# Kernel optimization log

Measured on AMD Instinct MI355X. Metric: run time of the kernel, lower is better.

Reference implementation:

```python
import jax, jax.numpy as jnp
import numpy as np

B, V, E, L, D = 4, 64, 1024, 1024, 256  # batch, vertices, edges/graph, seq_len, d_model
DEG = E // V


def setup_inputs() -> dict:
    key = jax.random.key(0)
    k0, k1, k2, k3, k4, k5 = jax.random.split(key, 6)
    # fixed 16-regular graph, edges sorted by (src, dst) so that nonzero()
    # extraction order of the dense adjacency equals a gather at (src, dst)
    src = np.repeat(np.arange(V), DEG)
    dst = (src + 1 + np.tile(np.arange(DEG), V)) % V
    order = np.lexsort((dst, src))
    src, dst = src[order], dst[order]
    edge_index = jnp.asarray(np.stack([np.tile(src, B), np.tile(dst, B)]), dtype=jnp.int32)
    hidden_states = jax.random.normal(k0, (B * V, L, D), dtype=jnp.float32)
    edge_weight = jax.random.uniform(k1, (B * E,), dtype=jnp.float32, minval=0.1, maxval=1.0)
    s = 0.02
    Wq = jax.random.normal(k2, (D, D), dtype=jnp.float32) * s
    bq = jax.random.normal(k3, (D,), dtype=jnp.float32) * s
    Wk = jax.random.normal(k4, (D, D), dtype=jnp.float32) * s
    bk = jax.random.normal(k5, (D,), dtype=jnp.float32) * s
    attn_skip = jnp.float32(0.5)
    return {"hidden_states": hidden_states, "edge_index": edge_index, "edge_weight": edge_weight,
            "Wq": Wq, "bq": bq, "Wk": Wk, "bk": bk, "attn_skip": attn_skip}


def reference(hidden_states, edge_index, edge_weight, Wq, bq, Wk, bk, attn_skip):
    # broadcast static edge list / weights across time, as the torch repeat does
    ei = jnp.broadcast_to(edge_index[:, :, None], (2, B * E, L))
    ew = jnp.broadcast_to(edge_weight[:, None], (B * E, L))
    hs = hidden_states.reshape(B, V, L, D)
    Q = hs @ Wq.T + bq  # nn.Linear: x W^T + b
    K = hs @ Wk.T + bk
    att = jnp.einsum('bvld,bwld->bvwl', Q, K) / jnp.sqrt(jnp.float32(D))
    bidx = jnp.repeat(jnp.arange(B), E)
    src, dst = edge_index[0], edge_index[1]
    # to_dense_adj: scatter-add edge weights -> (B, V, V, L)
    adj = jnp.zeros((B, V, V, L), att.dtype).at[bidx, src, dst, :].add(ew)
    mask = jnp.where(adj > 0, 0.0, -jnp.inf)
    att = jax.nn.softmax(att + mask, axis=2)  # softmax over destination vertices w
    adj_new = attn_skip * adj + (1.0 - attn_skip) * att
    # dense_to_sparse: nonzeros in (graph=b*L+l, row, col) row-major order.
    # Edges are sorted by (src,dst), so this is a gather; torch flat order is (b, l, e):
    g = adj_new[bidx, src, dst, :]  # (B*E, L) ordered (b, e, l)
    flat = g.reshape(B, E, L).transpose(0, 2, 1).reshape(-1)  # order (b, l, e)
    # replicate the original .view(B, E, L).transpose(1, 2).reshape(B*E, L)
    ew_out = flat.reshape(B, E, L).transpose(0, 2, 1).reshape(B * E, L)
    return ei, ew_out
```

## Files before the change

kernel.cpp:

```cpp
#include <hip/hip_runtime.h>
#include <cstdint>
#include <cstddef>

constexpr int Bv = 4;
constexpr int Vv = 64;
constexpr int Ev = 1024;
constexpr int Lv = 1024;
constexpr int BE = Bv * Ev;
constexpr size_t EI_PLANE = (size_t)BE * Lv;

constexpr int STRB = 264;

typedef __bf16 bf16x8 __attribute__((ext_vector_type(8)));
typedef __bf16 bf16x4 __attribute__((ext_vector_type(4)));
typedef float  f32x4  __attribute__((ext_vector_type(4)));

__global__ __launch_bounds__(64) void precompute_kernel(
    const float* __restrict__ Wq, const float* __restrict__ Wk,
    const float* __restrict__ bq, __bf16* __restrict__ Mb, float* __restrict__ rv)
{
    const int f = blockIdx.x;
    const int lane = threadIdx.x;
    if (f < 128) {
        const int k_tile = f >> 4;
        const int n_t    = f & 15;
        const int d0 = k_tile * 32 + (lane >> 4) * 8;
        const int t  = n_t * 16 + (lane & 15);
        float acc[8] = {0.f, 0.f, 0.f, 0.f, 0.f, 0.f, 0.f, 0.f};
        for (int i = 0; i < 256; ++i) {
            const float kv = Wk[i * 256 + t];
            const float4 q0 = *(const float4*)(Wq + i * 256 + d0);
            const float4 q1 = *(const float4*)(Wq + i * 256 + d0 + 4);
            acc[0] = fmaf(q0.x, kv, acc[0]);
            acc[1] = fmaf(q0.y, kv, acc[1]);
            acc[2] = fmaf(q0.z, kv, acc[2]);
            acc[3] = fmaf(q0.w, kv, acc[3]);
            acc[4] = fmaf(q1.x, kv, acc[4]);
            acc[5] = fmaf(q1.y, kv, acc[5]);
            acc[6] = fmaf(q1.z, kv, acc[6]);
            acc[7] = fmaf(q1.w, kv, acc[7]);
        }
        bf16x8 o;
        #pragma unroll
        for (int j = 0; j < 8; ++j) o[j] = (__bf16)acc[j];
        *(bf16x8*)(Mb + ((size_t)f * 64 + lane) * 8) = o;
    } else {
        #pragma unroll
        for (int q = 0; q < 4; ++q) {
            const int t = q * 64 + lane;
            float a0 = 0.f, a1 = 0.f;
            for (int i = 0; i < 256; i += 2) {
                a0 = fmaf(bq[i + 0], Wk[(i + 0) * 256 + t], a0);
                a1 = fmaf(bq[i + 1], Wk[(i + 1) * 256 + t], a1);
            }
            rv[t] = a0 + a1;
        }
    }
}

template <bool USE_WS>
__global__ __launch_bounds__(256) void edge_main(
    const float* __restrict__ hs, const int* __restrict__ eidx,
    const float* __restrict__ ew, const float* __restrict__ skipp,
    const __bf16* __restrict__ Mb, const float* __restrict__ rv,
    float* __restrict__ probs_or_out)
{
    __shared__ __bf16 hs_s[64 * STRB];
    __shared__ __bf16 T_s[64 * STRB];

    const int bl = blockIdx.x;
    const int b  = bl >> 10;
    const int l  = bl & 1023;
    const int tid  = threadIdx.x;
    const int w    = tid >> 6;
    const int lane = tid & 63;
    const int l15  = lane & 15;
    const int quad = lane >> 4;

    {
        const float* base = hs + ((size_t)b * 64 * 1024 + (size_t)l) * 256;
        const int c4 = (tid & 63) * 4;
        const int vo = tid >> 6;
        #pragma unroll
        for (int k = 0; k < 16; ++k) {
            const int v = k * 4 + vo;
            float4 val = *(const float4*)(base + (size_t)v * (1024 * 256) + c4);
            bf16x4 h;
            h[0] = (__bf16)val.x; h[1] = (__bf16)val.y;
            h[2] = (__bf16)val.z; h[3] = (__bf16)val.w;
            *(bf16x4*)(&hs_s[v * STRB + c4]) = h;
        }
    }
    __syncthreads();

    f32x4 acc[4][4];
    #pragma unroll
    for (int nt = 0; nt < 4; ++nt) {
        const float rb = rv[w * 64 + nt * 16 + l15];
        #pragma unroll
        for (int mt = 0; mt < 4; ++mt) {
            acc[mt][nt][0] = rb; acc[mt][nt][1] = rb;
            acc[mt][nt][2] = rb; acc[mt][nt][3] = rb;
        }
    }
    #pragma unroll
    for (int kt = 0; kt < 8; ++kt) {
        bf16x8 afr[4];
        #pragma unroll
        for (int mt = 0; mt < 4; ++mt)
            afr[mt] = *(const bf16x8*)(&hs_s[(mt * 16 + l15) * STRB + kt * 32 + quad * 8]);
        bf16x8 bfr[4];
        #pragma unroll
        for (int nt = 0; nt < 4; ++nt)
            bfr[nt] = *(const bf16x8*)(Mb + ((size_t)(kt * 16 + w * 4 + nt) * 64 + lane) * 8);
        #pragma unroll
        for (int mt = 0; mt < 4; ++mt)
            #pragma unroll
            for (int nt = 0; nt < 4; ++nt)
                acc[mt][nt] = __builtin_amdgcn_mfma_f32_16x16x32_bf16(
                    afr[mt], bfr[nt], acc[mt][nt], 0, 0, 0);
    }

    #pragma unroll
    for (int mt = 0; mt < 4; ++mt)
        #pragma unroll
        for (int nt = 0; nt < 4; ++nt)
            #pragma unroll
            for (int r = 0; r < 4; ++r) {
                const int row = mt * 16 + quad * 4 + r;
                const int col = w * 64 + nt * 16 + l15;
                T_s[row * STRB + col] = (__bf16)acc[mt][nt][r];
            }
    __syncthreads();

    f32x4 s_acc[4];
    #pragma unroll
    for (int nt = 0; nt < 4; ++nt) {
        s_acc[nt][0] = 0.f; s_acc[nt][1] = 0.f;
        s_acc[nt][2] = 0.f; s_acc[nt][3] = 0.f;
    }
    #pragma unroll
    for (int kt = 0; kt < 8; ++kt) {
        const bf16x8 afr = *(const bf16x8*)(&T_s[(w * 16 + l15) * STRB + kt * 32 + quad * 8]);
        #pragma unroll
        for (int nt = 0; nt < 4; ++nt) {
            const bf16x8 bfr = *(const bf16x8*)(&hs_s[(nt * 16 + l15) * STRB + kt * 32 + quad * 8]);
            s_acc[nt] = __builtin_amdgcn_mfma_f32_16x16x32_bf16(afr, bfr, s_acc[nt], 0, 0, 0);
        }
    }
    __syncthreads();

    float* S_s = (float*)hs_s;
    #pragma unroll
    for (int nt = 0; nt < 4; ++nt)
        #pragma unroll
        for (int r = 0; r < 4; ++r) {
            const int row = w * 16 + quad * 4 + r;
            const int col = nt * 16 + l15;
            S_s[row * 68 + col] = s_acc[nt][r] * 0.0625f;
        }
    __syncthreads();

    const int e0  = tid * 4;
    const int be0 = b * Ev + e0;
    int srcs[4], dsts[4];
    #pragma unroll
    for (int j = 0; j < 4; ++j) {
        srcs[j] = eidx[be0 + j];
        dsts[j] = eidx[BE + be0 + j];
    }
    float lg[4];
    #pragma unroll
    for (int j = 0; j < 4; ++j)
        lg[j] = S_s[srcs[j] * 68 + dsts[j]];

    float mx = fmaxf(fmaxf(lg[0], lg[1]), fmaxf(lg[2], lg[3]));
    mx = fmaxf(mx, __shfl_xor(mx, 1));
    mx = fmaxf(mx, __shfl_xor(mx, 2));
    float ex[4], sm = 0.f;
    #pragma unroll
    for (int j = 0; j < 4; ++j) { ex[j] = __expf(lg[j] - mx); sm += ex[j]; }
    sm += __shfl_xor(sm, 1);
    sm += __shfl_xor(sm, 2);
    const float inv = 1.0f / sm;

    if (USE_WS) {
        float4 o = make_float4(ex[0] * inv, ex[1] * inv, ex[2] * inv, ex[3] * inv);
        *(float4*)(probs_or_out + (size_t)bl * 1024 + e0) = o;
    } else {
        const float skip = skipp[0];
        const float om = 1.0f - skip;
        #pragma unroll
        for (int j = 0; j < 4; ++j) {
            float g = fmaf(skip, ew[be0 + j], om * (ex[j] * inv));
            probs_or_out[(size_t)(be0 + j) * Lv + l] = g;
        }
    }
}

__global__ __launch_bounds__(256) void output_kernel(
    const float* __restrict__ probs, const int* __restrict__ eidx,
    const float* __restrict__ ew, const float* __restrict__ skipp,
    float* __restrict__ out)
{
    __shared__ float tile[64 * 68];
    const int lt = blockIdx.x;
    const int et = blockIdx.y;
    const int b  = blockIdx.z;
    const int t  = threadIdx.x;
    const int tr = t >> 4;
    const int tc = t & 15;

    #pragma unroll
    for (int q = 0; q < 4; ++q) {
        const int lloc = q * 16 + tr;
        float4 v = *(const float4*)(probs +
            ((size_t)(b * 1024 + lt * 64 + lloc)) * 1024 + et * 64 + tc * 4);
        *(float4*)(&tile[lloc * 68 + tc * 4]) = v;
    }
    __syncthreads();

    const float skip = skipp[0];
    const float om = 1.0f - skip;
    float* out_ei0 = out;
    float* out_ei1 = out + EI_PLANE;
    float* out_ew  = out + 2 * EI_PLANE;

    #pragma unroll
    for (int q = 0; q < 4; ++q) {
        const int eloc = q * 16 + tr;
        const int be = b * Ev + et * 64 + eloc;
        const float w  = ew[be];
        const float sv = (float)eidx[be];
        const float dv = (float)eidx[BE + be];
        const int lloc0 = tc * 4;
        float4 o;
        o.x = fmaf(skip, w, om * tile[(lloc0 + 0) * 68 + eloc]);
        o.y = fmaf(skip, w, om * tile[(lloc0 + 1) * 68 + eloc]);
        o.z = fmaf(skip, w, om * tile[(lloc0 + 2) * 68 + eloc]);
        o.w = fmaf(skip, w, om * tile[(lloc0 + 3) * 68 + eloc]);
        const size_t off = (size_t)be * Lv + lt * 64 + lloc0;
        *(float4*)(out_ew  + off) = o;
        *(float4*)(out_ei0 + off) = make_float4(sv, sv, sv, sv);
        *(float4*)(out_ei1 + off) = make_float4(dv, dv, dv, dv);
    }
}

__global__ __launch_bounds__(256) void ei_kernel(
    const int* __restrict__ eidx, float* __restrict__ out)
{
    const int blk = blockIdx.x;
    const int c = blk >> 12;
    const int j = blk & 4095;
    const float v = (float)eidx[c * BE + j];
    float4 o = make_float4(v, v, v, v);
    *(float4*)(out + (size_t)blk * 1024 + threadIdx.x * 4) = o;
}

extern "C" void kernel_launch(void* const* d_in, const int* in_sizes, int n_in,
                              void* d_out, int out_size, void* d_ws, size_t ws_size,
                              hipStream_t stream)
{
    const float* hs   = (const float*)d_in[0];
    const int*   eidx = (const int*)d_in[1];
    const float* ew   = (const float*)d_in[2];
    const float* Wq   = (const float*)d_in[3];
    const float* bq   = (const float*)d_in[4];
    const float* Wk   = (const float*)d_in[5];
    const float* skip = (const float*)d_in[7];

    char* wsb = (char*)d_ws;
    __bf16* Mb   = (__bf16*)wsb;
    float*  rv   = (float*)(wsb + 131072);
    float*  probs = (float*)(wsb + 132096);
    const size_t need = 132096 + (size_t)Bv * Lv * Ev * sizeof(float);

    precompute_kernel<<<dim3(129), dim3(64), 0, stream>>>(Wq, Wk, bq, Mb, rv);

    if (ws_size >= need) {
        edge_main<true><<<dim3(Bv * Lv), dim3(256), 0, stream>>>(
            hs, eidx, ew, skip, Mb, rv, probs);
        output_kernel<<<dim3(16, 16, 4), dim3(256), 0, stream>>>(
            probs, eidx, ew, skip, (float*)d_out);
    } else {
        float* out_ew = (float*)d_out + 2 * EI_PLANE;
        edge_main<false><<<dim3(Bv * Lv), dim3(256), 0, stream>>>(
            hs, eidx, ew, skip, Mb, rv, out_ew);
        ei_kernel<<<dim3(2 * BE), dim3(256), 0, stream>>>(eidx, (float*)d_out);
    }
}
```

Before: 448.5 us.

## Chunk the T=hs·M GEMM into two column halves to shrink LDS and registers

The first GEMM (hs times the folded Wq^T·Wk matrix) is now computed in two 128-column chunks, each written to a smaller shared buffer and immediately consumed by the second GEMM. This halves the T tile in LDS and halves the accumulator registers, aiming for higher occupancy in the main per-(b,l) kernel. It also adds an extra barrier pair per chunk. The precompute kernel is rewritten to use 256-thread blocks with LDS-staged tiles, and it folds the 1/sqrt(D) scale into M and rv.

```diff
diff --git a/kernel.cpp b/kernel.cpp
--- a/kernel.cpp
+++ b/kernel.cpp
@@ -10,51 +10,57 @@
 constexpr size_t EI_PLANE = (size_t)BE * Lv;
 
 constexpr int STRB = 264;
+constexpr int TSTR = 136;
 
 typedef __bf16 bf16x8 __attribute__((ext_vector_type(8)));
 typedef __bf16 bf16x4 __attribute__((ext_vector_type(4)));
 typedef float  f32x4  __attribute__((ext_vector_type(4)));
 
-__global__ __launch_bounds__(64) void precompute_kernel(
+__global__ __launch_bounds__(256) void precompute_kernel(
     const float* __restrict__ Wq, const float* __restrict__ Wk,
     const float* __restrict__ bq, __bf16* __restrict__ Mb, float* __restrict__ rv)
 {
-    const int f = blockIdx.x;
-    const int lane = threadIdx.x;
-    if (f < 128) {
-        const int k_tile = f >> 4;
-        const int n_t    = f & 15;
-        const int d0 = k_tile * 32 + (lane >> 4) * 8;
-        const int t  = n_t * 16 + (lane & 15);
-        float acc[8] = {0.f, 0.f, 0.f, 0.f, 0.f, 0.f, 0.f, 0.f};
-        for (int i = 0; i < 256; ++i) {
-            const float kv = Wk[i * 256 + t];
-            const float4 q0 = *(const float4*)(Wq + i * 256 + d0);
-            const float4 q1 = *(const float4*)(Wq + i * 256 + d0 + 4);
-            acc[0] = fmaf(q0.x, kv, acc[0]);
-            acc[1] = fmaf(q0.y, kv, acc[1]);
-            acc[2] = fmaf(q0.z, kv, acc[2]);
-            acc[3] = fmaf(q0.w, kv, acc[3]);
-            acc[4] = fmaf(q1.x, kv, acc[4]);
-            acc[5] = fmaf(q1.y, kv, acc[5]);
-            acc[6] = fmaf(q1.z, kv, acc[6]);
-            acc[7] = fmaf(q1.w, kv, acc[7]);
-        }
-        bf16x8 o;
-        #pragma unroll
-        for (int j = 0; j < 8; ++j) o[j] = (__bf16)acc[j];
-        *(bf16x8*)(Mb + ((size_t)f * 64 + lane) * 8) = o;
+    const int blk = blockIdx.x;
+    const int tid = threadIdx.x;
+    if (blk < 256) {
+        __shared__ float qs[256 * 17];
+        __shared__ float ks[256 * 17];
+        const int i16 = (blk >> 4) * 16;
+        const int j16 = (blk & 15) * 16;
+        const int c  = tid & 15;
+        const int r0 = tid >> 4;
+        #pragma unroll
+        for (int it = 0; it < 16; ++it) {
+            const int r = it * 16 + r0;
+            qs[r * 17 + c] = Wq[r * 256 + i16 + c];
+            ks[r * 17 + c] = Wk[r * 256 + j16 + c];
+        }
+        __syncthreads();
+        const int dd = tid >> 4;
+        const int tt = tid & 15;
+        float a0 = 0.f, a1 = 0.f, a2 = 0.f, a3 = 0.f;
+        for (int r = 0; r < 256; r += 4) {
+            a0 = fmaf(qs[(r + 0) * 17 + dd], ks[(r + 0) * 17 + tt], a0);
+            a1 = fmaf(qs[(r + 1) * 17 + dd], ks[(r + 1) * 17 + tt], a1);
+            a2 = fmaf(qs[(r + 2) * 17 + dd], ks[(r + 2) * 17 + tt], a2);
+            a3 = fmaf(qs[(r + 3) * 17 + dd], ks[(r + 3) * 17 + tt], a3);
+        }
+        const float m = ((a0 + a1) + (a2 + a3)) * 0.0625f;
+        const int d = i16 + dd, t = j16 + tt;
+        const int f    = (d >> 5) * 16 + (t >> 4);
+        const int lane = ((d >> 3) & 3) * 16 + (t & 15);
+        const int jj   = d & 7;
+        Mb[((size_t)f * 64 + lane) * 8 + jj] = (__bf16)m;
     } else {
-        #pragma unroll
-        for (int q = 0; q < 4; ++q) {
-            const int t = q * 64 + lane;
-            float a0 = 0.f, a1 = 0.f;
-            for (int i = 0; i < 256; i += 2) {
-                a0 = fmaf(bq[i + 0], Wk[(i + 0) * 256 + t], a0);
-                a1 = fmaf(bq[i + 1], Wk[(i + 1) * 256 + t], a1);
-            }
-            rv[t] = a0 + a1;
-        }
+        __shared__ float bqs[256];
+        bqs[tid] = bq[tid];
+        __syncthreads();
+        float a0 = 0.f, a1 = 0.f;
+        for (int i = 0; i < 256; i += 2) {
+            a0 = fmaf(bqs[i + 0], Wk[(i + 0) * 256 + tid], a0);
+            a1 = fmaf(bqs[i + 1], Wk[(i + 1) * 256 + tid], a1);
+        }
+        rv[tid] = (a0 + a1) * 0.0625f;
     }
 }
 
@@ -66,7 +72,9 @@
     float* __restrict__ probs_or_out)
 {
     __shared__ __bf16 hs_s[64 * STRB];
-    __shared__ __bf16 T_s[64 * STRB];
+    __shared__ float  Tbuf[64 * TSTR / 2];
+    __bf16* T16 = (__bf16*)Tbuf;
+    float*  S_s = Tbuf;
 
     const int bl = blockIdx.x;
     const int b  = bl >> 10;
@@ -93,72 +101,71 @@
     }
     __syncthreads();
 
-    f32x4 acc[4][4];
-    #pragma unroll
-    for (int nt = 0; nt < 4; ++nt) {
-        const float rb = rv[w * 64 + nt * 16 + l15];
-        #pragma unroll
-        for (int mt = 0; mt < 4; ++mt) {
-            acc[mt][nt][0] = rb; acc[mt][nt][1] = rb;
-            acc[mt][nt][2] = rb; acc[mt][nt][3] = rb;
-        }
-    }
-    #pragma unroll
-    for (int kt = 0; kt < 8; ++kt) {
-        bf16x8 afr[4];
-        #pragma unroll
-        for (int mt = 0; mt < 4; ++mt)
-            afr[mt] = *(const bf16x8*)(&hs_s[(mt * 16 + l15) * STRB + kt * 32 + quad * 8]);
-        bf16x8 bfr[4];
-        #pragma unroll
-        for (int nt = 0; nt < 4; ++nt)
-            bfr[nt] = *(const bf16x8*)(Mb + ((size_t)(kt * 16 + w * 4 + nt) * 64 + lane) * 8);
-        #pragma unroll
-        for (int mt = 0; mt < 4; ++mt)
-            #pragma unroll
-            for (int nt = 0; nt < 4; ++nt)
-                acc[mt][nt] = __builtin_amdgcn_mfma_f32_16x16x32_bf16(
-                    afr[mt], bfr[nt], acc[mt][nt], 0, 0, 0);
-    }
-
-    #pragma unroll
-    for (int mt = 0; mt < 4; ++mt)
-        #pragma unroll
-        for (int nt = 0; nt < 4; ++nt)
-            #pragma unroll
-            for (int r = 0; r < 4; ++r) {
-                const int row = mt * 16 + quad * 4 + r;
-                const int col = w * 64 + nt * 16 + l15;
-                T_s[row * STRB + col] = (__bf16)acc[mt][nt][r];
-            }
-    __syncthreads();
-
     f32x4 s_acc[4];
     #pragma unroll
     for (int nt = 0; nt < 4; ++nt) {
         s_acc[nt][0] = 0.f; s_acc[nt][1] = 0.f;
         s_acc[nt][2] = 0.f; s_acc[nt][3] = 0.f;
     }
-    #pragma unroll
-    for (int kt = 0; kt < 8; ++kt) {
-        const bf16x8 afr = *(const bf16x8*)(&T_s[(w * 16 + l15) * STRB + kt * 32 + quad * 8]);
-        #pragma unroll
-        for (int nt = 0; nt < 4; ++nt) {
-            const bf16x8 bfr = *(const bf16x8*)(&hs_s[(nt * 16 + l15) * STRB + kt * 32 + quad * 8]);
-            s_acc[nt] = __builtin_amdgcn_mfma_f32_16x16x32_bf16(afr, bfr, s_acc[nt], 0, 0, 0);
-        }
-    }
-    __syncthreads();
-
-    float* S_s = (float*)hs_s;
+
+    #pragma unroll
+    for (int cch = 0; cch < 2; ++cch) {
+        f32x4 acc[4][2];
+        #pragma unroll
+        for (int nt = 0; nt < 2; ++nt) {
+            const float rb = rv[cch * 128 + w * 32 + nt * 16 + l15];
+            #pragma unroll
+            for (int mt = 0; mt < 4; ++mt) {
+                acc[mt][nt][0] = rb; acc[mt][nt][1] = rb;
+                acc[mt][nt][2] = rb; acc[mt][nt][3] = rb;
+            }
+        }
+        #pragma unroll
+        for (int kt = 0; kt < 8; ++kt) {
+            bf16x8 afr[4];
+            #pragma unroll
+            for (int mt = 0; mt < 4; ++mt)
+                afr[mt] = *(const bf16x8*)(&hs_s[(mt * 16 + l15) * STRB + kt * 32 + quad * 8]);
+            bf16x8 bfr[2];
+            #pragma unroll
+            for (int nt = 0; nt < 2; ++nt)
+                bfr[nt] = *(const bf16x8*)(Mb +
+                    ((size_t)(kt * 16 + cch * 8 + w * 2 + nt) * 64 + lane) * 8);
+            #pragma unroll
+            for (int mt = 0; mt < 4; ++mt)
+                #pragma unroll
+                for (int nt = 0; nt < 2; ++nt)
+                    acc[mt][nt] = __builtin_amdgcn_mfma_f32_16x16x32_bf16(
+                        afr[mt], bfr[nt], acc[mt][nt], 0, 0, 0);
+        }
+        #pragma unroll
+        for (int mt = 0; mt < 4; ++mt)
+            #pragma unroll
+            for (int nt = 0; nt < 2; ++nt)
+                #pragma unroll
+                for (int r = 0; r < 4; ++r)
+                    T16[(mt * 16 + quad * 4 + r) * TSTR + w * 32 + nt * 16 + l15] =
+                        (__bf16)acc[mt][nt][r];
+        __syncthreads();
+
+        #pragma unroll
+        for (int kt2 = 0; kt2 < 4; ++kt2) {
+            const bf16x8 afr = *(const bf16x8*)(&T16[(w * 16 + l15) * TSTR + kt2 * 32 + quad * 8]);
+            #pragma unroll
+            for (int nt = 0; nt < 4; ++nt) {
+                const bf16x8 bfr = *(const bf16x8*)(
+                    &hs_s[(nt * 16 + l15) * STRB + cch * 128 + kt2 * 32 + quad * 8]);
+                s_acc[nt] = __builtin_amdgcn_mfma_f32_16x16x32_bf16(afr, bfr, s_acc[nt], 0, 0, 0);
+            }
+        }
+        __syncthreads();
+    }
+
     #pragma unroll
     for (int nt = 0; nt < 4; ++nt)
         #pragma unroll
-        for (int r = 0; r < 4; ++r) {
-            const int row = w * 16 + quad * 4 + r;
-            const int col = nt * 16 + l15;
-            S_s[row * 68 + col] = s_acc[nt][r] * 0.0625f;
-        }
+        for (int r = 0; r < 4; ++r)
+            S_s[(w * 16 + quad * 4 + r) * 68 + nt * 16 + l15] = s_acc[nt][r];
     __syncthreads();
 
     const int e0  = tid * 4;
@@ -275,7 +282,7 @@
     float*  probs = (float*)(wsb + 132096);
     const size_t need = 132096 + (size_t)Bv * Lv * Ev * sizeof(float);
 
-    precompute_kernel<<<dim3(129), dim3(64), 0, stream>>>(Wq, Wk, bq, Mb, rv);
+    precompute_kernel<<<dim3(257), dim3(256), 0, stream>>>(Wq, Wk, bq, Mb, rv);
 
     if (ws_size >= need) {
         edge_main<true><<<dim3(Bv * Lv), dim3(256), 0, stream>>>(
```

Result: faster. 425.4 us (-5.1%).
